# Performance work log

Hardware: AMD Instinct MI355X
Metric: run time of the kernel (lower is better)

## Reference

```python
import jax, jax.numpy as jnp
import numpy as np

Q, N, H, C, L = 512, 1000, 1024, 128, 8  # questions, students, hidden, concepts, lstm layers
LAM, GUESS = 10.0, 0.25  # self.l and guess_prob


def setup_inputs() -> dict:
    key = jax.random.key(0)
    ks = jax.random.split(key, 12)
    def w(k, shape, fan):
        return (jax.random.uniform(k, shape, jnp.float32, -1.0, 1.0) / np.sqrt(fan)).astype(jnp.float32)
    return {
        "inputs": jax.random.normal(ks[0], (Q, N), jnp.float32),
        "concept_col": jax.random.randint(ks[1], (Q,), 0, C),  # concepts[1][i]
        "W_inp": w(ks[2], (H, N), N),
        "b_inp": jnp.zeros((H,), jnp.float32),
        "W_ih0": w(ks[3], (4 * N, H), H),
        "W_hh0": w(ks[4], (4 * N, N), N),
        "b_ih0": jnp.zeros((4 * N,), jnp.float32),
        "b_hh0": jnp.zeros((4 * N,), jnp.float32),
        "W_ih": w(ks[5], (L - 1, 4 * N, N), N),
        "W_hh": w(ks[6], (L - 1, 4 * N, N), N),
        "b_ih": jnp.zeros((L - 1, 4 * N), jnp.float32),
        "b_hh": jnp.zeros((L - 1, 4 * N), jnp.float32),
        "W_lin": w(ks[7], (C,), 1),  # Linear(1, C) weight, shape [C]
        "b_lin": jnp.zeros((C,), jnp.float32),
        "D_nz": 0.1 * jax.random.normal(ks[8], (Q,), jnp.float32),  # D[concepts]
    }


def _cell(Wih, Whh, bih, bhh, x, h, c):
    # PyTorch LSTM cell, gate order i,f,g,o
    g = Wih @ x + bih + Whh @ h + bhh
    i, f, gg, o = jnp.split(g, 4)
    i, f, o = jax.nn.sigmoid(i), jax.nn.sigmoid(f), jax.nn.sigmoid(o)
    c = f * c + i * jnp.tanh(gg)
    return o * jnp.tanh(c), c


def _forward(inputs, concept_col, W_inp, b_inp, W_ih0, W_hh0, b_ih0, b_hh0,
             W_ih, W_hh, b_ih, b_hh, W_lin, b_lin, D_nz):
    def step(carry, xs):
        h, c, ssum = carry  # h,c: [L,N]
        x_row, cc, d = xs
        x = W_inp @ x_row + b_inp  # [H]
        hs, cs = [], []
        hl, cl = _cell(W_ih0, W_hh0, b_ih0, b_hh0, x, h[0], c[0])
        hs.append(hl); cs.append(cl)
        for l in range(L - 1):
            hl, cl = _cell(W_ih[l], W_hh[l], b_ih[l], b_hh[l], hl, h[l + 1], c[l + 1])
            hs.append(hl); cs.append(cl)
        skills = hl[:, None] * W_lin[None, :] + b_lin  # [N, C]
        skills = (skills - skills.min()) / (skills.max() - skills.min())  # global min-max
        out = jnp.maximum(GUESS, 1.0 - jnp.exp(-LAM * (skills[:, cc] - d)))  # floored_exp_irf, [N]
        return (jnp.stack(hs), jnp.stack(cs), ssum + skills), out

    h0 = jnp.zeros((L, N), inputs.dtype)
    c0 = jnp.zeros((L, N), inputs.dtype)
    s0 = jnp.zeros((N, C), inputs.dtype)
    (h, c, ssum), outputs = jax.lax.scan(step, (h0, c0, s0), (inputs, concept_col, D_nz))
    return outputs, ssum / Q  # outputs [Q,N], averaged skills [N,C]


def reference(inputs, concept_col, W_inp, b_inp, W_ih0, W_hh0, b_ih0, b_hh0,
              W_ih, W_hh, b_ih, b_hh, W_lin, b_lin, D_nz):
    return _forward(inputs, concept_col, W_inp, b_inp, W_ih0, W_hh0, b_ih0, b_hh0,
                    W_ih, W_hh, b_ih, b_hh, W_lin, b_lin, D_nz)
```

## Files before the change

kernel.cpp:

```cpp
#include <hip/hip_runtime.h>
#include <math.h>

#define QQ 512
#define NN 1000
#define HHID 1024
#define HPAD 1024
#define CCON 128
#define G4 4000
#define LAYERS 8
#define TC 64
#define CHUNKS (QQ / TC)
#define CONC 4
#define LBLK 63

typedef unsigned long long ull;

__device__ inline float wred_min(float v){ for(int o=32;o;o>>=1) v=fminf(v,__shfl_xor(v,o)); return v; }
__device__ inline float wred_max(float v){ for(int o=32;o;o>>=1) v=fmaxf(v,__shfl_xor(v,o)); return v; }
__device__ inline float wred_sum(float v){ for(int o=32;o;o>>=1) v+=__shfl_xor(v,o); return v; }

__global__ __launch_bounds__(256) void gemm_nt(
    const float* __restrict__ A, const float* __restrict__ B,
    const float* __restrict__ bias1,
    float* __restrict__ C, int M, int K, int R, int lda, int ldc) {
  __shared__ float As[16][65];
  __shared__ float Bs[16][65];
  int tid = threadIdx.x;
  int tx = tid & 15, ty = tid >> 4;
  int m0 = blockIdx.y * 64, r0 = blockIdx.x * 64;
  float acc[4][4] = {};
  for (int k0 = 0; k0 < K; k0 += 16) {
#pragma unroll
    for (int i = 0; i < 4; i++) {
      int idx = tid + 256 * i;
      int ml = idx >> 4, kl = idx & 15;
      int m = m0 + ml, k = k0 + kl;
      As[kl][ml] = (m < M && k < K) ? A[(size_t)m * lda + k] : 0.f;
      int r = r0 + ml;
      Bs[kl][ml] = (r < R && k < K) ? B[(size_t)r * K + k] : 0.f;
    }
    __syncthreads();
#pragma unroll
    for (int kk = 0; kk < 16; kk++) {
      float a[4], b[4];
#pragma unroll
      for (int i = 0; i < 4; i++) a[i] = As[kk][ty * 4 + i];
#pragma unroll
      for (int j = 0; j < 4; j++) b[j] = Bs[kk][tx * 4 + j];
#pragma unroll
      for (int i = 0; i < 4; i++)
#pragma unroll
        for (int j = 0; j < 4; j++) acc[i][j] += a[i] * b[j];
    }
    __syncthreads();
  }
#pragma unroll
  for (int i = 0; i < 4; i++) {
    int m = m0 + ty * 4 + i;
    if (m >= M) continue;
#pragma unroll
    for (int j = 0; j < 4; j++) {
      int r = r0 + tx * 4 + j;
      if (r >= R) continue;
      float v = acc[i][j];
      if (bias1) v += bias1[r];
      C[(size_t)m * ldc + r] = v;
    }
  }
}

struct RPair { const float* HinF;
               const ull* Hin64;
               const float* Wih; const float* b1; const float* b2;
               const float* Whh; ull* Hout64;
               float* Call; int t0; int kin; };
struct RArgs { RPair p[CONC]; };

__global__ __launch_bounds__(1024, 4) void lstm_stage(RArgs args) {
  RPair rp = args.p[blockIdx.y];
  __shared__ __align__(16) float As[64][68];
  __shared__ __align__(16) float Bs[64][68];
  __shared__ float gl[TC * 64];
  __shared__ float hs[2][1024];
  int tid = threadIdx.x;
  int wave = tid >> 6, lane = tid & 63;
  int n = blockIdx.x * 16 + wave;
  bool active = (n < NN);
  int kin = rp.kin;
  int t0 = rp.t0;

  if (tid >= NN) { hs[0][tid] = 0.f; hs[1][tid] = 0.f; }

  {
    int ttA = tid >> 4;
    int w16 = tid & 15;
    int nn = blockIdx.x * 16 + w16;
    float accq[4] = {0.f, 0.f, 0.f, 0.f};
    float pbq[4];
#pragma unroll
    for (int q = 0; q < 4; q++)
      pbq[q] = (nn < NN) ? rp.b1[q * NN + nn] + rp.b2[q * NN + nn] : 0.f;
    int ldr = tid >> 4, ldc4 = tid & 15;
    int qb = ldr >> 4, nb = blockIdx.x * 16 + (ldr & 15);
    for (int k0 = 0; k0 < kin; k0 += 64) {
      int k = k0 + ldc4 * 4;
      float4 av;
      if (kin == HHID) {
        av = *(const float4*)&rp.HinF[(size_t)(t0 + ldr) * HPAD + k];
      } else if (k + 3 < kin) {
        const ull* p = &rp.Hin64[(size_t)(t0 + ldr) * HPAD + k];
        ulonglong2 u0 = *(const ulonglong2*)&p[0];
        ulonglong2 u1 = *(const ulonglong2*)&p[2];
        av.x = __uint_as_float((unsigned)u0.x);
        av.y = __uint_as_float((unsigned)u0.y);
        av.z = __uint_as_float((unsigned)u1.x);
        av.w = __uint_as_float((unsigned)u1.y);
      } else {
        float* f = (float*)&av;
#pragma unroll
        for (int e = 0; e < 4; e++)
          f[e] = (k + e < kin)
              ? __uint_as_float(
                    (unsigned)rp.Hin64[(size_t)(t0 + ldr) * HPAD + k + e])
              : 0.f;
      }
      *(float4*)&As[ldr][ldc4 * 4] = av;
      float4 bv = {0.f, 0.f, 0.f, 0.f};
      if (nb < NN) {
        if (k + 3 < kin) {
          bv = *(const float4*)&rp.Wih[(size_t)(qb * NN + nb) * kin + k];
        } else {
          float* f = (float*)&bv;
#pragma unroll
          for (int e = 0; e < 4; e++)
            if (k + e < kin)
              f[e] = rp.Wih[(size_t)(qb * NN + nb) * kin + k + e];
        }
      }
      *(float4*)&Bs[ldr][ldc4 * 4] = bv;
      __syncthreads();
#pragma unroll
      for (int kk = 0; kk < 64; kk += 4) {
        float4 a = *(const float4*)&As[ttA][kk];
#pragma unroll
        for (int q = 0; q < 4; q++) {
          float4 b = *(const float4*)&Bs[q * 16 + w16][kk];
          accq[q] += a.x * b.x + a.y * b.y + a.z * b.z + a.w * b.w;
        }
      }
      __syncthreads();
    }
#pragma unroll
    for (int q = 0; q < 4; q++)
      gl[ttA * 64 + q * 16 + w16] = accq[q] + pbq[q];
  }

  float wreg[4][16];
  if (active) {
#pragma unroll
    for (int q = 0; q < 4; q++) {
      const float* wr = rp.Whh + (size_t)(q * NN + n) * NN;
#pragma unroll
      for (int it = 0; it < 16; it++) {
        int k = it * 64 + lane;
        wreg[q][it] = (k < NN) ? wr[k] : 0.f;
      }
    }
  } else {
#pragma unroll
    for (int q = 0; q < 4; q++)
#pragma unroll
      for (int it = 0; it < 16; it++) wreg[q][it] = 0.f;
  }
#pragma unroll
  for (int q = 0; q < 4; q++)
#pragma unroll
    for (int it = 0; it < 16; it++)
      asm volatile("" : "+v"(wreg[q][it]));

  __syncthreads();

  float creg = 0.f;
  if (t0 > 0 && active) creg = rp.Call[n];

  for (int tt = 0; tt < TC; tt++) {
    int t = t0 + tt;
    float* hb = hs[t & 1];
    if (t > 0 && tid < NN) {
      const ull* src = rp.Hout64 + (size_t)(t - 1) * HPAD + tid;
      for (;;) {
        ull v = __hip_atomic_load(src, __ATOMIC_RELAXED,
                                  __HIP_MEMORY_SCOPE_AGENT);
        if ((unsigned)(v >> 32) == (unsigned)t) {
          hb[tid] = __uint_as_float((unsigned)v);
          break;
        }
        __builtin_amdgcn_s_sleep(1);
      }
    }
    __syncthreads();
    if (active) {
      float g0 = gl[tt * 64 + wave];
      float g1 = gl[tt * 64 + 16 + wave];
      float g2 = gl[tt * 64 + 32 + wave];
      float g3 = gl[tt * 64 + 48 + wave];
      if (t > 0) {
        float a0 = 0.f, a1 = 0.f, a2 = 0.f, a3 = 0.f;
#pragma unroll
        for (int it = 0; it < 16; it++) {
          float hv = hb[it * 64 + lane];
          a0 += wreg[0][it] * hv;
          a1 += wreg[1][it] * hv;
          a2 += wreg[2][it] * hv;
          a3 += wreg[3][it] * hv;
        }
#pragma unroll
        for (int o = 32; o; o >>= 1) {
          a0 += __shfl_xor(a0, o);
          a1 += __shfl_xor(a1, o);
          a2 += __shfl_xor(a2, o);
          a3 += __shfl_xor(a3, o);
        }
        g0 += a0; g1 += a1; g2 += a2; g3 += a3;
      }
      float ii = 1.f / (1.f + expf(-g0));
      float ff = 1.f / (1.f + expf(-g1));
      float gg = tanhf(g2);
      float oo = 1.f / (1.f + expf(-g3));
      creg = ff * creg + ii * gg;
      float h = oo * tanhf(creg);
      if (lane == 0) {
        ull pkt = ((ull)(unsigned)(t + 1) << 32) | (ull)__float_as_uint(h);
        __hip_atomic_store(&rp.Hout64[(size_t)t * HPAD + n], pkt,
                           __ATOMIC_RELAXED, __HIP_MEMORY_SCOPE_AGENT);
      }
    }
  }
  if (active && lane == 0)
    __hip_atomic_store(&rp.Call[n], creg, __ATOMIC_RELAXED,
                       __HIP_MEMORY_SCOPE_AGENT);
}

__global__ __launch_bounds__(256) void epilogue_out(
    const ull* __restrict__ H7,
    const float* __restrict__ Wlin, const float* __restrict__ blin,
    const int* __restrict__ ccol, const float* __restrict__ Dnz,
    float* __restrict__ out,
    float* __restrict__ irbuf, float* __restrict__ mnirbuf) {
  int t = blockIdx.x, tid = threadIdx.x;
  int wave = tid >> 6, lane = tid & 63;
  __shared__ float hbuf[NN];
  __shared__ float smin[4], smax[4];
  __shared__ float bc[2];
  float lmin = 3.4e38f, lmax = -3.4e38f;
  for (int i = tid; i < NN; i += 256) {
    float v = __uint_as_float((unsigned)H7[(size_t)t * HPAD + i]);
    hbuf[i] = v;
    lmin = fminf(lmin, v); lmax = fmaxf(lmax, v);
  }
  lmin = wred_min(lmin); lmax = wred_max(lmax);
  if (lane == 0) { smin[wave] = lmin; smax[wave] = lmax; }
  __syncthreads();
  if (tid == 0) {
    bc[0] = fminf(fminf(smin[0], smin[1]), fminf(smin[2], smin[3]));
    bc[1] = fmaxf(fmaxf(smax[0], smax[1]), fmaxf(smax[2], smax[3]));
  }
  __syncthreads();
  float hmn = bc[0], hmx = bc[1];
  float clo = 3.4e38f, chi = -3.4e38f;
  if (tid < CCON) {
    float w = Wlin[tid], b = blin[tid];
    clo = b + fminf(w * hmn, w * hmx);
    chi = b + fmaxf(w * hmn, w * hmx);
  }
  clo = wred_min(clo); chi = wred_max(chi);
  __syncthreads();
  if (lane == 0) { smin[wave] = clo; smax[wave] = chi; }
  __syncthreads();
  if (tid == 0) {
    float mn = fminf(fminf(smin[0], smin[1]), fminf(smin[2], smin[3]));
    float mx = fmaxf(fmaxf(smax[0], smax[1]), fmaxf(smax[2], smax[3]));
    float ir = 1.f / (mx - mn);
    bc[0] = mn; bc[1] = ir;
    irbuf[t] = ir;
    mnirbuf[t] = mn * ir;
  }
  __syncthreads();
  float mn = bc[0], ir = bc[1];
  int cc = ccol[t];
  float wcc = Wlin[cc], bcc = blin[cc], d = Dnz[t];
  for (int n = tid; n < NN; n += 256) {
    float s = (hbuf[n] * wcc + bcc - mn) * ir;
    out[(size_t)t * NN + n] = fmaxf(0.25f, 1.f - expf(-10.f * (s - d)));
  }
}

__global__ void reduce_scalars(const float* __restrict__ ir,
                               const float* __restrict__ mnir,
                               float* __restrict__ scal) {
  int tid = threadIdx.x;
  int wave = tid >> 6, lane = tid & 63;
  __shared__ float s1[8], s2[8];
  float a = ir[tid], b = mnir[tid];
  a = wred_sum(a); b = wred_sum(b);
  if (lane == 0) { s1[wave] = a; s2[wave] = b; }
  __syncthreads();
  if (tid == 0) {
    float A = 0.f, B = 0.f;
    for (int i = 0; i < 8; i++) { A += s1[i]; B += s2[i]; }
    scal[0] = A; scal[1] = B;
  }
}

__global__ void accum_A(const ull* __restrict__ H7,
                        const float* __restrict__ ir,
                        float* __restrict__ Avec) {
  int n = blockIdx.x * 256 + threadIdx.x;
  if (n < NN) {
    float acc = 0.f;
    for (int t = 0; t < QQ; t++)
      acc += __uint_as_float((unsigned)H7[(size_t)t * HPAD + n]) * ir[t];
    Avec[n] = acc;
  }
}

__global__ void skills_out(const float* __restrict__ Avec,
                           const float* __restrict__ Wlin,
                           const float* __restrict__ blin,
                           const float* __restrict__ scal,
                           float* __restrict__ out) {
  int idx = blockIdx.x * 256 + threadIdx.x;
  if (idx < NN * CCON) {
    int n = idx >> 7, c = idx & 127;
    out[idx] = (Wlin[c] * Avec[n] + blin[c] * scal[0] - scal[1]) * (1.f / (float)QQ);
  }
}

extern "C" void kernel_launch(void* const* d_in, const int* in_sizes, int n_in,
                              void* d_out, int out_size, void* d_ws, size_t ws_size,
                              hipStream_t stream) {
  const float* inputs = (const float*)d_in[0];
  const int*   ccol   = (const int*)d_in[1];
  const float* W_inp  = (const float*)d_in[2];
  const float* b_inp  = (const float*)d_in[3];
  const float* W_ih0  = (const float*)d_in[4];
  const float* W_hh0  = (const float*)d_in[5];
  const float* b_ih0  = (const float*)d_in[6];
  const float* b_hh0  = (const float*)d_in[7];
  const float* W_ih   = (const float*)d_in[8];
  const float* W_hh   = (const float*)d_in[9];
  const float* b_ih   = (const float*)d_in[10];
  const float* b_hh   = (const float*)d_in[11];
  const float* W_lin  = (const float*)d_in[12];
  const float* b_lin  = (const float*)d_in[13];
  const float* D_nz   = (const float*)d_in[14];

  float* ws = (float*)d_ws;
  float* X     = ws;
  ull*   Hall  = (ull*)(X + (size_t)QQ * HPAD);
  float* tail  = (float*)(Hall + (size_t)LAYERS * QQ * HPAD);
  float* Call  = tail;
  float* irb   = Call + LAYERS * HPAD;
  float* mnir  = irb + QQ;
  float* Avec  = mnir + QQ;
  float* scal  = Avec + 1024;

  float* out_main   = (float*)d_out;
  float* out_skills = (float*)d_out + QQ * NN;

  hipMemsetAsync(Hall, 0, (size_t)LAYERS * QQ * HPAD * sizeof(ull), stream);

  gemm_nt<<<dim3(HPAD / 64, QQ / 64), 256, 0, stream>>>(
      inputs, W_inp, b_inp, X, QQ, NN, HPAD, NN, HPAD);

  bool donep[LAYERS][CHUNKS] = {};
  int remaining = LAYERS * CHUNKS;
  while (remaining > 0) {
    int pl[CONC], pcid[CONC];
    bool sel[LAYERS][CHUNKS] = {};
    int np = 0;
    for (int pick = 0; pick < CONC; pick++) {
      int bl = -1, bc = -1, bkey = 1 << 30;
      for (int l = 0; l < LAYERS; l++)
        for (int c = 0; c < CHUNKS; c++) {
          if (donep[l][c] || sel[l][c]) continue;
          if (l > 0 && !donep[l - 1][c]) continue;
          if (c > 0 && !donep[l][c - 1]) continue;
          int key = (l + c) * 16 + (LAYERS - 1 - l);
          if (key < bkey) { bkey = key; bl = l; bc = c; }
        }
      if (bl < 0) break;
      sel[bl][bc] = true; pl[np] = bl; pcid[np] = bc; np++;
    }
    RArgs ra;
    for (int i = 0; i < np; i++) {
      int l = pl[i], c = pcid[i];
      RPair& r = ra.p[i];
      if (l == 0) {
        r.HinF = X; r.Hin64 = nullptr;
        r.Wih = W_ih0; r.b1 = b_ih0; r.b2 = b_hh0;
        r.Whh = W_hh0; r.kin = HHID;
      } else {
        r.HinF = nullptr;
        r.Hin64 = Hall + (size_t)(l - 1) * QQ * HPAD;
        r.Wih = W_ih + (size_t)(l - 1) * G4 * NN;
        r.b1 = b_ih + (size_t)(l - 1) * G4;
        r.b2 = b_hh + (size_t)(l - 1) * G4;
        r.Whh = W_hh + (size_t)(l - 1) * G4 * NN;
        r.kin = NN;
      }
      r.Hout64 = Hall + (size_t)l * QQ * HPAD;
      r.Call = Call + l * HPAD;
      r.t0 = c * TC;
    }
    for (int i = np; i < CONC; i++) ra.p[i] = ra.p[0];
    lstm_stage<<<dim3(LBLK, np), 1024, 0, stream>>>(ra);
    for (int i = 0; i < np; i++) donep[pl[i]][pcid[i]] = true;
    remaining -= np;
  }

  const ull* H7 = Hall + (size_t)7 * QQ * HPAD;
  epilogue_out<<<QQ, 256, 0, stream>>>(H7, W_lin, b_lin, ccol, D_nz,
                                       out_main, irb, mnir);
  reduce_scalars<<<1, 512, 0, stream>>>(irb, mnir, scal);
  accum_A<<<4, 256, 0, stream>>>(H7, irb, Avec);
  skills_out<<<(NN * CCON) / 256, 256, 0, stream>>>(Avec, W_lin, b_lin, scal,
                                                    out_skills);
}
```

Baseline: 6.806 ms.

## Replace per-stage LSTM launches with one persistent kernel using flag-based sync

The host-side wavefront schedule of (layer, chunk) tiles was issued as many separate lstm_stage launches. It is now encoded into the kernel arguments and run by a single persistent lstm_persist launch. Cross-stage dependencies are enforced on the device by spinning on tagged h packets and tagged cell-state packets. This removes the kernel launch gaps and the implicit grid barriers between stages, so work from different stages can overlap. The cost is busy-wait polling and atomic per-element loads for the input projection, and it relies on all 252 blocks being co-resident to avoid deadlock.

```diff
diff --git a/kernel.cpp b/kernel.cpp
--- a/kernel.cpp
+++ b/kernel.cpp
@@ -12,6 +12,7 @@
 #define CHUNKS (QQ / TC)
 #define CONC 4
 #define LBLK 63
+#define MAXSTG 32
 
 typedef unsigned long long ull;
 
@@ -69,176 +70,217 @@
   }
 }
 
-struct RPair { const float* HinF;
-               const ull* Hin64;
-               const float* Wih; const float* b1; const float* b2;
-               const float* Whh; ull* Hout64;
-               float* Call; int t0; int kin; };
-struct RArgs { RPair p[CONC]; };
-
-__global__ __launch_bounds__(1024, 4) void lstm_stage(RArgs args) {
-  RPair rp = args.p[blockIdx.y];
+struct PArgs {
+  const float* X;
+  const float* Wih0; const float* Whh0; const float* bih0; const float* bhh0;
+  const float* Wih7; const float* Whh7; const float* bih7; const float* bhh7;
+  ull* Hall; ull* Call64;
+  int nstages;
+  int pl[MAXSTG * CONC]; int pc[MAXSTG * CONC];
+};
+
+__global__ __launch_bounds__(1024, 4) void lstm_persist(PArgs a) {
   __shared__ __align__(16) float As[64][68];
   __shared__ __align__(16) float Bs[64][68];
   __shared__ float gl[TC * 64];
   __shared__ float hs[2][1024];
+  int blkid = blockIdx.x;
+  int lanePair = blockIdx.y;
   int tid = threadIdx.x;
   int wave = tid >> 6, lane = tid & 63;
-  int n = blockIdx.x * 16 + wave;
+  int n = blkid * 16 + wave;
   bool active = (n < NN);
-  int kin = rp.kin;
-  int t0 = rp.t0;
 
   if (tid >= NN) { hs[0][tid] = 0.f; hs[1][tid] = 0.f; }
-
-  {
-    int ttA = tid >> 4;
-    int w16 = tid & 15;
-    int nn = blockIdx.x * 16 + w16;
-    float accq[4] = {0.f, 0.f, 0.f, 0.f};
-    float pbq[4];
+  __syncthreads();
+
+  for (int s = 0; s < a.nstages; s++) {
+    int l = a.pl[s * CONC + lanePair];
+    if (l < 0) continue;
+    int c = a.pc[s * CONC + lanePair];
+    int t0 = c * TC;
+    int kin = (l == 0) ? HHID : NN;
+    const float* Wih = (l == 0) ? a.Wih0 : a.Wih7 + (size_t)(l - 1) * G4 * NN;
+    const float* Whh = (l == 0) ? a.Whh0 : a.Whh7 + (size_t)(l - 1) * G4 * NN;
+    const float* b1  = (l == 0) ? a.bih0 : a.bih7 + (size_t)(l - 1) * G4;
+    const float* b2  = (l == 0) ? a.bhh0 : a.bhh7 + (size_t)(l - 1) * G4;
+    const ull* Hin64 = a.Hall + (size_t)(l - 1) * QQ * HPAD;
+    ull* Hout64 = a.Hall + (size_t)l * QQ * HPAD;
+    ull* CallL = a.Call64 + (size_t)l * HPAD;
+
+    if (l > 0) {
+      if (tid < NN) {
+        const ull* gp = &Hin64[(size_t)(t0 + TC - 1) * HPAD + tid];
+        while ((unsigned)(__hip_atomic_load(gp, __ATOMIC_RELAXED,
+                                            __HIP_MEMORY_SCOPE_AGENT) >> 32)
+               != (unsigned)(t0 + TC))
+          __builtin_amdgcn_s_sleep(8);
+      }
+      __syncthreads();
+    }
+
+    {
+      int ttA = tid >> 4;
+      int w16 = tid & 15;
+      int nn = blkid * 16 + w16;
+      float accq[4] = {0.f, 0.f, 0.f, 0.f};
+      float pbq[4];
+#pragma unroll
+      for (int q = 0; q < 4; q++)
+        pbq[q] = (nn < NN) ? b1[q * NN + nn] + b2[q * NN + nn] : 0.f;
+      int ldr = tid >> 4, ldc4 = tid & 15;
+      int qb = ldr >> 4, nb = blkid * 16 + (ldr & 15);
+      for (int k0 = 0; k0 < kin; k0 += 64) {
+        int k = k0 + ldc4 * 4;
+        float4 av;
+        if (l == 0) {
+          av = *(const float4*)&a.X[(size_t)(t0 + ldr) * HPAD + k];
+        } else {
+          float f0 = 0.f, f1 = 0.f, f2 = 0.f, f3 = 0.f;
+          const ull* rowp = &Hin64[(size_t)(t0 + ldr) * HPAD];
+          if (k < kin)
+            f0 = __uint_as_float((unsigned)__hip_atomic_load(
+                &rowp[k], __ATOMIC_RELAXED, __HIP_MEMORY_SCOPE_AGENT));
+          if (k + 1 < kin)
+            f1 = __uint_as_float((unsigned)__hip_atomic_load(
+                &rowp[k + 1], __ATOMIC_RELAXED, __HIP_MEMORY_SCOPE_AGENT));
+          if (k + 2 < kin)
+            f2 = __uint_as_float((unsigned)__hip_atomic_load(
+                &rowp[k + 2], __ATOMIC_RELAXED, __HIP_MEMORY_SCOPE_AGENT));
+          if (k + 3 < kin)
+            f3 = __uint_as_float((unsigned)__hip_atomic_load(
+                &rowp[k + 3], __ATOMIC_RELAXED, __HIP_MEMORY_SCOPE_AGENT));
+          av.x = f0; av.y = f1; av.z = f2; av.w = f3;
+        }
+        *(float4*)&As[ldr][ldc4 * 4] = av;
+        float4 bv = {0.f, 0.f, 0.f, 0.f};
+        if (nb < NN) {
+          if (k + 3 < kin) {
+            bv = *(const float4*)&Wih[(size_t)(qb * NN + nb) * kin + k];
+          } else {
+            float* f = (float*)&bv;
+#pragma unroll
+            for (int e = 0; e < 4; e++)
+              if (k + e < kin) f[e] = Wih[(size_t)(qb * NN + nb) * kin + k + e];
+          }
+        }
+        *(float4*)&Bs[ldr][ldc4 * 4] = bv;
+        __syncthreads();
+#pragma unroll
+        for (int kk = 0; kk < 64; kk += 4) {
+          float4 aa = *(const float4*)&As[ttA][kk];
+#pragma unroll
+          for (int q = 0; q < 4; q++) {
+            float4 b = *(const float4*)&Bs[q * 16 + w16][kk];
+            accq[q] += aa.x * b.x + aa.y * b.y + aa.z * b.z + aa.w * b.w;
+          }
+        }
+        __syncthreads();
+      }
+#pragma unroll
+      for (int q = 0; q < 4; q++)
+        gl[ttA * 64 + q * 16 + w16] = accq[q] + pbq[q];
+    }
+
+    float wreg[4][16];
+    if (active) {
+#pragma unroll
+      for (int q = 0; q < 4; q++) {
+        const float* wr = Whh + (size_t)(q * NN + n) * NN;
+#pragma unroll
+        for (int it = 0; it < 16; it++) {
+          int k = it * 64 + lane;
+          wreg[q][it] = (k < NN) ? wr[k] : 0.f;
+        }
+      }
+    } else {
+#pragma unroll
+      for (int q = 0; q < 4; q++)
+#pragma unroll
+        for (int it = 0; it < 16; it++) wreg[q][it] = 0.f;
+    }
 #pragma unroll
     for (int q = 0; q < 4; q++)
-      pbq[q] = (nn < NN) ? rp.b1[q * NN + nn] + rp.b2[q * NN + nn] : 0.f;
-    int ldr = tid >> 4, ldc4 = tid & 15;
-    int qb = ldr >> 4, nb = blockIdx.x * 16 + (ldr & 15);
-    for (int k0 = 0; k0 < kin; k0 += 64) {
-      int k = k0 + ldc4 * 4;
-      float4 av;
-      if (kin == HHID) {
-        av = *(const float4*)&rp.HinF[(size_t)(t0 + ldr) * HPAD + k];
-      } else if (k + 3 < kin) {
-        const ull* p = &rp.Hin64[(size_t)(t0 + ldr) * HPAD + k];
-        ulonglong2 u0 = *(const ulonglong2*)&p[0];
-        ulonglong2 u1 = *(const ulonglong2*)&p[2];
-        av.x = __uint_as_float((unsigned)u0.x);
-        av.y = __uint_as_float((unsigned)u0.y);
-        av.z = __uint_as_float((unsigned)u1.x);
-        av.w = __uint_as_float((unsigned)u1.y);
-      } else {
-        float* f = (float*)&av;
-#pragma unroll
-        for (int e = 0; e < 4; e++)
-          f[e] = (k + e < kin)
-              ? __uint_as_float(
-                    (unsigned)rp.Hin64[(size_t)(t0 + ldr) * HPAD + k + e])
-              : 0.f;
-      }
-      *(float4*)&As[ldr][ldc4 * 4] = av;
-      float4 bv = {0.f, 0.f, 0.f, 0.f};
-      if (nb < NN) {
-        if (k + 3 < kin) {
-          bv = *(const float4*)&rp.Wih[(size_t)(qb * NN + nb) * kin + k];
-        } else {
-          float* f = (float*)&bv;
-#pragma unroll
-          for (int e = 0; e < 4; e++)
-            if (k + e < kin)
-              f[e] = rp.Wih[(size_t)(qb * NN + nb) * kin + k + e];
-        }
-      }
-      *(float4*)&Bs[ldr][ldc4 * 4] = bv;
+#pragma unroll
+      for (int it = 0; it < 16; it++)
+        asm volatile("" : "+v"(wreg[q][it]));
+
+    __syncthreads();
+
+    float creg = 0.f;
+    if (t0 > 0 && active) {
+      const ull* cp = &CallL[n];
+      for (;;) {
+        ull v = __hip_atomic_load(cp, __ATOMIC_RELAXED,
+                                  __HIP_MEMORY_SCOPE_AGENT);
+        if ((unsigned)(v >> 32) == (unsigned)c) {
+          creg = __uint_as_float((unsigned)v);
+          break;
+        }
+        __builtin_amdgcn_s_sleep(2);
+      }
+    }
+
+    for (int tt = 0; tt < TC; tt++) {
+      int t = t0 + tt;
+      float* hb = hs[t & 1];
+      if (t > 0 && tid < NN) {
+        const ull* src = Hout64 + (size_t)(t - 1) * HPAD + tid;
+        for (;;) {
+          ull v = __hip_atomic_load(src, __ATOMIC_RELAXED,
+                                    __HIP_MEMORY_SCOPE_AGENT);
+          if ((unsigned)(v >> 32) == (unsigned)t) {
+            hb[tid] = __uint_as_float((unsigned)v);
+            break;
+          }
+          __builtin_amdgcn_s_sleep(1);
+        }
+      }
       __syncthreads();
-#pragma unroll
-      for (int kk = 0; kk < 64; kk += 4) {
-        float4 a = *(const float4*)&As[ttA][kk];
-#pragma unroll
-        for (int q = 0; q < 4; q++) {
-          float4 b = *(const float4*)&Bs[q * 16 + w16][kk];
-          accq[q] += a.x * b.x + a.y * b.y + a.z * b.z + a.w * b.w;
-        }
-      }
-      __syncthreads();
-    }
-#pragma unroll
-    for (int q = 0; q < 4; q++)
-      gl[ttA * 64 + q * 16 + w16] = accq[q] + pbq[q];
-  }
-
-  float wreg[4][16];
-  if (active) {
-#pragma unroll
-    for (int q = 0; q < 4; q++) {
-      const float* wr = rp.Whh + (size_t)(q * NN + n) * NN;
-#pragma unroll
-      for (int it = 0; it < 16; it++) {
-        int k = it * 64 + lane;
-        wreg[q][it] = (k < NN) ? wr[k] : 0.f;
-      }
-    }
-  } else {
-#pragma unroll
-    for (int q = 0; q < 4; q++)
-#pragma unroll
-      for (int it = 0; it < 16; it++) wreg[q][it] = 0.f;
-  }
-#pragma unroll
-  for (int q = 0; q < 4; q++)
-#pragma unroll
-    for (int it = 0; it < 16; it++)
-      asm volatile("" : "+v"(wreg[q][it]));
-
-  __syncthreads();
-
-  float creg = 0.f;
-  if (t0 > 0 && active) creg = rp.Call[n];
-
-  for (int tt = 0; tt < TC; tt++) {
-    int t = t0 + tt;
-    float* hb = hs[t & 1];
-    if (t > 0 && tid < NN) {
-      const ull* src = rp.Hout64 + (size_t)(t - 1) * HPAD + tid;
-      for (;;) {
-        ull v = __hip_atomic_load(src, __ATOMIC_RELAXED,
-                                  __HIP_MEMORY_SCOPE_AGENT);
-        if ((unsigned)(v >> 32) == (unsigned)t) {
-          hb[tid] = __uint_as_float((unsigned)v);
-          break;
-        }
-        __builtin_amdgcn_s_sleep(1);
-      }
+      if (active) {
+        float g0 = gl[tt * 64 + wave];
+        float g1 = gl[tt * 64 + 16 + wave];
+        float g2 = gl[tt * 64 + 32 + wave];
+        float g3 = gl[tt * 64 + 48 + wave];
+        if (t > 0) {
+          float a0 = 0.f, a1 = 0.f, a2 = 0.f, a3 = 0.f;
+#pragma unroll
+          for (int it = 0; it < 16; it++) {
+            float hv = hb[it * 64 + lane];
+            a0 += wreg[0][it] * hv;
+            a1 += wreg[1][it] * hv;
+            a2 += wreg[2][it] * hv;
+            a3 += wreg[3][it] * hv;
+          }
+#pragma unroll
+          for (int o = 32; o; o >>= 1) {
+            a0 += __shfl_xor(a0, o);
+            a1 += __shfl_xor(a1, o);
+            a2 += __shfl_xor(a2, o);
+            a3 += __shfl_xor(a3, o);
+          }
+          g0 += a0; g1 += a1; g2 += a2; g3 += a3;
+        }
+        float ii = 1.f / (1.f + expf(-g0));
+        float ff = 1.f / (1.f + expf(-g1));
+        float gg = tanhf(g2);
+        float oo = 1.f / (1.f + expf(-g3));
+        creg = ff * creg + ii * gg;
+        float h = oo * tanhf(creg);
+        if (lane == 0) {
+          ull pkt = ((ull)(unsigned)(t + 1) << 32) | (ull)__float_as_uint(h);
+          __hip_atomic_store(&Hout64[(size_t)t * HPAD + n], pkt,
+                             __ATOMIC_RELAXED, __HIP_MEMORY_SCOPE_AGENT);
+        }
+      }
+    }
+    if (active && lane == 0) {
+      ull pkt = ((ull)(unsigned)(c + 1) << 32) | (ull)__float_as_uint(creg);
+      __hip_atomic_store(&CallL[n], pkt, __ATOMIC_RELAXED,
+                         __HIP_MEMORY_SCOPE_AGENT);
     }
     __syncthreads();
-    if (active) {
-      float g0 = gl[tt * 64 + wave];
-      float g1 = gl[tt * 64 + 16 + wave];
-      float g2 = gl[tt * 64 + 32 + wave];
-      float g3 = gl[tt * 64 + 48 + wave];
-      if (t > 0) {
-        float a0 = 0.f, a1 = 0.f, a2 = 0.f, a3 = 0.f;
-#pragma unroll
-        for (int it = 0; it < 16; it++) {
-          float hv = hb[it * 64 + lane];
-          a0 += wreg[0][it] * hv;
-          a1 += wreg[1][it] * hv;
-          a2 += wreg[2][it] * hv;
-          a3 += wreg[3][it] * hv;
-        }
-#pragma unroll
-        for (int o = 32; o; o >>= 1) {
-          a0 += __shfl_xor(a0, o);
-          a1 += __shfl_xor(a1, o);
-          a2 += __shfl_xor(a2, o);
-          a3 += __shfl_xor(a3, o);
-        }
-        g0 += a0; g1 += a1; g2 += a2; g3 += a3;
-      }
-      float ii = 1.f / (1.f + expf(-g0));
-      float ff = 1.f / (1.f + expf(-g1));
-      float gg = tanhf(g2);
-      float oo = 1.f / (1.f + expf(-g3));
-      creg = ff * creg + ii * gg;
-      float h = oo * tanhf(creg);
-      if (lane == 0) {
-        ull pkt = ((ull)(unsigned)(t + 1) << 32) | (ull)__float_as_uint(h);
-        __hip_atomic_store(&rp.Hout64[(size_t)t * HPAD + n], pkt,
-                           __ATOMIC_RELAXED, __HIP_MEMORY_SCOPE_AGENT);
-      }
-    }
-  }
-  if (active && lane == 0)
-    __hip_atomic_store(&rp.Call[n], creg, __ATOMIC_RELAXED,
-                       __HIP_MEMORY_SCOPE_AGENT);
+  }
 }
 
 __global__ __launch_bounds__(256) void epilogue_out(
@@ -358,9 +400,9 @@
   float* ws = (float*)d_ws;
   float* X     = ws;
   ull*   Hall  = (ull*)(X + (size_t)QQ * HPAD);
-  float* tail  = (float*)(Hall + (size_t)LAYERS * QQ * HPAD);
-  float* Call  = tail;
-  float* irb   = Call + LAYERS * HPAD;
+  ull*   Call64 = Hall + (size_t)LAYERS * QQ * HPAD;
+  float* tail  = (float*)(Call64 + (size_t)LAYERS * HPAD);
+  float* irb   = tail;
   float* mnir  = irb + QQ;
   float* Avec  = mnir + QQ;
   float* scal  = Avec + 1024;
@@ -368,56 +410,51 @@
   float* out_main   = (float*)d_out;
   float* out_skills = (float*)d_out + QQ * NN;
 
-  hipMemsetAsync(Hall, 0, (size_t)LAYERS * QQ * HPAD * sizeof(ull), stream);
+  hipMemsetAsync(Hall, 0,
+                 ((size_t)LAYERS * QQ * HPAD + LAYERS * HPAD) * sizeof(ull),
+                 stream);
 
   gemm_nt<<<dim3(HPAD / 64, QQ / 64), 256, 0, stream>>>(
       inputs, W_inp, b_inp, X, QQ, NN, HPAD, NN, HPAD);
 
-  bool donep[LAYERS][CHUNKS] = {};
-  int remaining = LAYERS * CHUNKS;
-  while (remaining > 0) {
-    int pl[CONC], pcid[CONC];
-    bool sel[LAYERS][CHUNKS] = {};
-    int np = 0;
-    for (int pick = 0; pick < CONC; pick++) {
-      int bl = -1, bc = -1, bkey = 1 << 30;
-      for (int l = 0; l < LAYERS; l++)
-        for (int c = 0; c < CHUNKS; c++) {
-          if (donep[l][c] || sel[l][c]) continue;
-          if (l > 0 && !donep[l - 1][c]) continue;
-          if (c > 0 && !donep[l][c - 1]) continue;
-          int key = (l + c) * 16 + (LAYERS - 1 - l);
-          if (key < bkey) { bkey = key; bl = l; bc = c; }
-        }
-      if (bl < 0) break;
-      sel[bl][bc] = true; pl[np] = bl; pcid[np] = bc; np++;
-    }
-    RArgs ra;
-    for (int i = 0; i < np; i++) {
-      int l = pl[i], c = pcid[i];
-      RPair& r = ra.p[i];
-      if (l == 0) {
-        r.HinF = X; r.Hin64 = nullptr;
-        r.Wih = W_ih0; r.b1 = b_ih0; r.b2 = b_hh0;
-        r.Whh = W_hh0; r.kin = HHID;
-      } else {
-        r.HinF = nullptr;
-        r.Hin64 = Hall + (size_t)(l - 1) * QQ * HPAD;
-        r.Wih = W_ih + (size_t)(l - 1) * G4 * NN;
-        r.b1 = b_ih + (size_t)(l - 1) * G4;
-        r.b2 = b_hh + (size_t)(l - 1) * G4;
-        r.Whh = W_hh + (size_t)(l - 1) * G4 * NN;
-        r.kin = NN;
-      }
-      r.Hout64 = Hall + (size_t)l * QQ * HPAD;
-      r.Call = Call + l * HPAD;
-      r.t0 = c * TC;
-    }
-    for (int i = np; i < CONC; i++) ra.p[i] = ra.p[0];
-    lstm_stage<<<dim3(LBLK, np), 1024, 0, stream>>>(ra);
-    for (int i = 0; i < np; i++) donep[pl[i]][pcid[i]] = true;
-    remaining -= np;
-  }
+  PArgs pa;
+  pa.X = X;
+  pa.Wih0 = W_ih0; pa.Whh0 = W_hh0; pa.bih0 = b_ih0; pa.bhh0 = b_hh0;
+  pa.Wih7 = W_ih; pa.Whh7 = W_hh; pa.bih7 = b_ih; pa.bhh7 = b_hh;
+  pa.Hall = Hall; pa.Call64 = Call64;
+  for (int i = 0; i < MAXSTG * CONC; i++) { pa.pl[i] = -1; pa.pc[i] = -1; }
+  {
+    bool donep[LAYERS][CHUNKS] = {};
+    int remaining = LAYERS * CHUNKS;
+    int s = 0;
+    while (remaining > 0 && s < MAXSTG) {
+      bool sel[LAYERS][CHUNKS] = {};
+      int np = 0;
+      int spl[CONC], spc[CONC];
+      for (int pick = 0; pick < CONC; pick++) {
+        int bl = -1, bc = -1, bkey = 1 << 30;
+        for (int l = 0; l < LAYERS; l++)
+          for (int c = 0; c < CHUNKS; c++) {
+            if (donep[l][c] || sel[l][c]) continue;
+            if (l > 0 && !donep[l - 1][c]) continue;
+            if (c > 0 && !donep[l][c - 1]) continue;
+            int key = (l + c) * 16 + (LAYERS - 1 - l);
+            if (key < bkey) { bkey = key; bl = l; bc = c; }
+          }
+        if (bl < 0) break;
+        sel[bl][bc] = true; spl[np] = bl; spc[np] = bc; np++;
+      }
+      for (int i = 0; i < np; i++) {
+        pa.pl[s * CONC + i] = spl[i];
+        pa.pc[s * CONC + i] = spc[i];
+        donep[spl[i]][spc[i]] = true;
+      }
+      remaining -= np;
+      s++;
+    }
+    pa.nstages = s;
+  }
+  lstm_persist<<<dim3(LBLK, CONC), 1024, 0, stream>>>(pa);
 
   const ull* H7 = Hall + (size_t)7 * QQ * HPAD;
   epilogue_out<<<QQ, 256, 0, stream>>>(H7, W_lin, b_lin, ccol, D_nz,
```

Result: slower. 7.200 ms (+5.8%).
